# Optimization experiments

Hardware: AMD Instinct MI355X
Metric: run time of the kernel (lower is better)

The kernel has to match this reference:

```python
import jax, jax.numpy as jnp
import numpy as np

B, C_IN, C_OUT, T, R, CO = 8, 64, 64, 32, 32, 32


def setup_inputs() -> dict:
    key = jax.random.key(0)
    ks = jax.random.split(key, 8)
    scale = 1.0 / np.sqrt(C_IN)  # nn.Linear default uniform(-1/sqrt(in), 1/sqrt(in))
    w = lambda k: jax.random.uniform(k, (C_OUT, C_IN), jnp.float32, -scale, scale)
    return {
        "x": jax.random.normal(ks[0], (B, C_IN, T, R, CO), jnp.float32),
        "w_self": w(ks[1]),
        "w_tp": w(ks[2]),
        "w_tm": w(ks[3]),
        "w_rp": w(ks[4]),
        "w_rm": w(ks[5]),
        "w_cp": w(ks[6]),
        "w_cm": w(ks[7]),
    }


def _proj(v, w):
    # v: [B, t, r, c, C_in], w: [C_out, C_in] (nn.Linear layout)
    return jnp.einsum('btrci,oi->btrco', v, w)


def _shift_pad(a, axis, front):
    # pad 1 slice at front (True) or back (False) along `axis` of a 5-D tensor
    pads = [(0, 0)] * 5
    pads[axis] = (1, 0) if front else (0, 1)
    return jnp.pad(a, pads)


def reference(x, w_self, w_tp, w_tm, w_rp, w_rm, w_cp, w_cm):
    xp = jnp.transpose(x, (0, 2, 3, 4, 1))  # [B, T, R, Co, C_in]
    out = _proj(xp, w_self)
    if xp.shape[1] > 1:
        out = out + _shift_pad(_proj(xp[:, :-1], w_tp), 1, True)
        out = out + _shift_pad(_proj(xp[:, 1:], w_tm), 1, False)
    if xp.shape[2] > 1:
        out = out + _shift_pad(_proj(xp[:, :, :-1], w_rp), 2, True)
        out = out + _shift_pad(_proj(xp[:, :, 1:], w_rm), 2, False)
    if xp.shape[3] > 1:
        out = out + _shift_pad(_proj(xp[:, :, :, :-1], w_cp), 3, True)
        out = out + _shift_pad(_proj(xp[:, :, :, 1:], w_cm), 3, False)
    return jnp.transpose(out, (0, 4, 1, 2, 3))  # [B, C_out, T, R, Co]
```

## Files before the change

kernel.cpp:

```cpp
#include <hip/hip_runtime.h>


#define SB 32768
#define CIN 64
#define COUT 64
#define NB 8

typedef short s16x8 __attribute__((ext_vector_type(8)));
typedef __bf16 bf16x8 __attribute__((ext_vector_type(8)));
typedef float f32x4 __attribute__((ext_vector_type(4)));

__device__ __forceinline__ unsigned f2bf(float f) {
    unsigned u = __float_as_uint(f);
    u += 0x7FFFu + ((u >> 16) & 1u);
    return u >> 16;
}
__device__ __forceinline__ unsigned pk2(float lo, float hi) {
    return f2bf(lo) | (f2bf(hi) << 16);
}

__global__ __launch_bounds__(256) void wprep_kernel(const float* __restrict__ w0,
                            const float* __restrict__ w1, const float* __restrict__ w2,
                            const float* __restrict__ w3, const float* __restrict__ w4,
                            const float* __restrict__ w5, const float* __restrict__ w6,
                            unsigned short* __restrict__ ws) {
    int tap = blockIdx.x;
    int tid = threadIdx.x;
    const float* w = (tap == 0) ? w0 : (tap == 1) ? w1 : (tap == 2) ? w2
                   : (tap == 3) ? w3 : (tap == 4) ? w4 : (tap == 5) ? w5 : w6;
    unsigned p[8];
#pragma unroll
    for (int j = 0; j < 8; ++j)
        p[j] = pk2(w[tid * 16 + 2 * j], w[tid * 16 + 2 * j + 1]);
    uint4* dp = (uint4*)(ws + tap * 4096 + tid * 16);
    dp[0] = make_uint4(p[0], p[1], p[2], p[3]);
    dp[1] = make_uint4(p[4], p[5], p[6], p[7]);
}

__global__ __launch_bounds__(256) void conv_kernel(const float* __restrict__ x,
                                                   const unsigned short* __restrict__ wq,
                                                   float* __restrict__ out) {
    __shared__ uint4 alds[1536];
    int bid = blockIdx.x;
    int b = bid >> 8;
    int sblk = (bid & 255) << 7;
    int tid = threadIdx.x;
    const float* xb = x + (size_t)b * CIN * SB;

    {
        int row = tid & 127;
        int half = tid >> 7;
        int rl = 32 + row;
        const float* xp = xb + sblk + row + (size_t)(half * 32) * SB;
        unsigned pk[16];
#pragma unroll
        for (int u = 0; u < 16; ++u)
            pk[u] = pk2(xp[(size_t)(2 * u) * SB], xp[(size_t)(2 * u + 1) * SB]);
#pragma unroll
        for (int j = 0; j < 4; ++j)
            alds[rl * 8 + ((half * 4 + j) ^ (rl & 7))] =
                make_uint4(pk[4 * j], pk[4 * j + 1], pk[4 * j + 2], pk[4 * j + 3]);
    }
    {
        int hrow = tid & 63;
        int rl = (hrow < 32) ? hrow : hrow + 128;
        int s = sblk - 32 + rl;
        s = max(0, min(SB - 1, s));
        int ic = tid >> 6;
        const float* xp = xb + s + (size_t)(ic * 16) * SB;
        unsigned pk[8];
#pragma unroll
        for (int u = 0; u < 8; ++u)
            pk[u] = pk2(xp[(size_t)(2 * u) * SB], xp[(size_t)(2 * u + 1) * SB]);
        alds[rl * 8 + ((2 * ic) ^ (rl & 7))] = make_uint4(pk[0], pk[1], pk[2], pk[3]);
        alds[rl * 8 + ((2 * ic + 1) ^ (rl & 7))] = make_uint4(pk[4], pk[5], pk[6], pk[7]);
    }
    __syncthreads();

    int lane = tid & 63;
    int wv = tid >> 6;
    int lo = lane & 15;
    int quad = lane >> 4;
    int sbase = sblk + wv * 32;
    int t = sblk >> 10;

    f32x4 acc[2][4];
#pragma unroll
    for (int mt = 0; mt < 2; ++mt)
#pragma unroll
        for (int nt = 0; nt < 4; ++nt)
            acc[mt][nt] = (f32x4){0.f, 0.f, 0.f, 0.f};

    int r_m[2], c_m[2], rl[2];
#pragma unroll
    for (int mt = 0; mt < 2; ++mt) {
        int s = sbase + mt * 16 + lo;
        r_m[mt] = (s >> 5) & 31;
        c_m[mt] = s & 31;
        rl[mt] = s - sblk + 32;
    }

    auto load_b = [&](const unsigned short* wt, int ks, int nt) -> bf16x8 {
        const unsigned short* bp = wt + (nt * 16 + lo) * 64 + ks * 32 + quad * 8;
        return __builtin_bit_cast(bf16x8, *(const s16x8*)bp);
    };

    auto run_tap_lds = [&](int tap, int d, const bool ok[2]) {
        const unsigned short* wt = wq + tap * 4096;
#pragma unroll
        for (int ks = 0; ks < 2; ++ks) {
            bf16x8 bf[4];
#pragma unroll
            for (int nt = 0; nt < 4; ++nt) bf[nt] = load_b(wt, ks, nt);
            int j = ks * 4 + quad;
#pragma unroll
            for (int mt = 0; mt < 2; ++mt) {
                int row = rl[mt] + d;
                s16x8 raw = *((const s16x8*)alds + row * 8 + (j ^ (row & 7)));
                s16x8 zz = {0, 0, 0, 0, 0, 0, 0, 0};
                raw = ok[mt] ? raw : zz;
                bf16x8 af = __builtin_bit_cast(bf16x8, raw);
#pragma unroll
                for (int nt = 0; nt < 4; ++nt)
                    acc[mt][nt] = __builtin_amdgcn_mfma_f32_16x16x32_bf16(af, bf[nt], acc[mt][nt], 0, 0, 0);
            }
        }
    };

    auto run_tap_gather = [&](int tap, int d) {
        const unsigned short* wt = wq + tap * 4096;
#pragma unroll
        for (int ks = 0; ks < 2; ++ks) {
            bf16x8 bf[4];
#pragma unroll
            for (int nt = 0; nt < 4; ++nt) bf[nt] = load_b(wt, ks, nt);
            const float* gp = xb + (size_t)(ks * 32 + quad * 8) * SB + d;
#pragma unroll
            for (int mt = 0; mt < 2; ++mt) {
                const float* ap = gp + sbase + mt * 16 + lo;
                unsigned pk[4];
#pragma unroll
                for (int u = 0; u < 4; ++u)
                    pk[u] = pk2(ap[(size_t)(2 * u) * SB], ap[(size_t)(2 * u + 1) * SB]);
                uint4 v = make_uint4(pk[0], pk[1], pk[2], pk[3]);
                bf16x8 af = __builtin_bit_cast(bf16x8, v);
#pragma unroll
                for (int nt = 0; nt < 4; ++nt)
                    acc[mt][nt] = __builtin_amdgcn_mfma_f32_16x16x32_bf16(af, bf[nt], acc[mt][nt], 0, 0, 0);
            }
        }
    };

    {
        bool ok_all[2] = {true, true};
        run_tap_lds(0, 0, ok_all);
    }
    if (t > 0)  run_tap_gather(1, -1024);
    if (t < 31) run_tap_gather(2, 1024);
    {
        bool ok[2];
#pragma unroll
        for (int mt = 0; mt < 2; ++mt) ok[mt] = (r_m[mt] > 0);
        run_tap_lds(3, -32, ok);
#pragma unroll
        for (int mt = 0; mt < 2; ++mt) ok[mt] = (r_m[mt] < 31);
        run_tap_lds(4, 32, ok);
#pragma unroll
        for (int mt = 0; mt < 2; ++mt) ok[mt] = (c_m[mt] > 0);
        run_tap_lds(5, -1, ok);
#pragma unroll
        for (int mt = 0; mt < 2; ++mt) ok[mt] = (c_m[mt] < 31);
        run_tap_lds(6, 1, ok);
    }

#pragma unroll
    for (int mt = 0; mt < 2; ++mt) {
#pragma unroll
        for (int nt = 0; nt < 4; ++nt) {
            int o = nt * 16 + lo;
            size_t off = ((size_t)(b * COUT + o)) * SB + sbase + mt * 16 + quad * 4;
            *(f32x4*)(out + off) = acc[mt][nt];
        }
    }
}

__global__ void fallback_kernel(const float* __restrict__ x,
                                const float* __restrict__ w0, const float* __restrict__ w1,
                                const float* __restrict__ w2, const float* __restrict__ w3,
                                const float* __restrict__ w4, const float* __restrict__ w5,
                                const float* __restrict__ w6,
                                float* __restrict__ out) {
    int bid = blockIdx.x;
    int b = bid >> 11;
    int og = (bid >> 7) & 15;
    int sblk = (bid & 127) << 8;
    int tid = threadIdx.x;
    __shared__ float wl[7][4][64];
    const float* wp[7] = {w0, w1, w2, w3, w4, w5, w6};
    for (int k = tid; k < 7 * 4 * 64; k += 256) {
        int tap = k >> 8, oo = (k >> 6) & 3, i = k & 63;
        wl[tap][oo][i] = wp[tap][(og * 4 + oo) * 64 + i];
    }
    __syncthreads();
    int s = sblk + tid;
    int t = s >> 10, r = (s >> 5) & 31, c = s & 31;
    const float* xb = x + (size_t)b * CIN * SB + s;
    float a0 = 0, a1 = 0, a2 = 0, a3 = 0;
    for (int i = 0; i < 64; ++i) {
        const float* xi = xb + (size_t)i * SB;
        float vs = xi[0];
        float vtp = (t > 0) ? xi[-1024] : 0.f;
        float vtm = (t < 31) ? xi[1024] : 0.f;
        float vrp = (r > 0) ? xi[-32] : 0.f;
        float vrm = (r < 31) ? xi[32] : 0.f;
        float vcp = (c > 0) ? xi[-1] : 0.f;
        float vcm = (c < 31) ? xi[1] : 0.f;
        a0 += wl[0][0][i] * vs + wl[1][0][i] * vtp + wl[2][0][i] * vtm + wl[3][0][i] * vrp + wl[4][0][i] * vrm + wl[5][0][i] * vcp + wl[6][0][i] * vcm;
        a1 += wl[0][1][i] * vs + wl[1][1][i] * vtp + wl[2][1][i] * vtm + wl[3][1][i] * vrp + wl[4][1][i] * vrm + wl[5][1][i] * vcp + wl[6][1][i] * vcm;
        a2 += wl[0][2][i] * vs + wl[1][2][i] * vtp + wl[2][2][i] * vtm + wl[3][2][i] * vrp + wl[4][2][i] * vrm + wl[5][2][i] * vcp + wl[6][2][i] * vcm;
        a3 += wl[0][3][i] * vs + wl[1][3][i] * vtp + wl[2][3][i] * vtm + wl[3][3][i] * vrp + wl[4][3][i] * vrm + wl[5][3][i] * vcp + wl[6][3][i] * vcm;
    }
    size_t obase = ((size_t)b * COUT + og * 4) * SB + s;
    out[obase] = a0;
    out[obase + SB] = a1;
    out[obase + 2 * (size_t)SB] = a2;
    out[obase + 3 * (size_t)SB] = a3;
}

extern "C" void kernel_launch(void* const* d_in, const int* in_sizes, int n_in,
                              void* d_out, int out_size, void* d_ws, size_t ws_size,
                              hipStream_t stream) {
    const float* x = (const float*)d_in[0];
    const float* w0 = (const float*)d_in[1];
    const float* w1 = (const float*)d_in[2];
    const float* w2 = (const float*)d_in[3];
    const float* w3 = (const float*)d_in[4];
    const float* w4 = (const float*)d_in[5];
    const float* w5 = (const float*)d_in[6];
    const float* w6 = (const float*)d_in[7];
    float* out = (float*)d_out;

    size_t need = (size_t)7 * 4096 * 2;
    if (d_ws != nullptr && ws_size >= need) {
        unsigned short* wsp = (unsigned short*)d_ws;
        wprep_kernel<<<7, 256, 0, stream>>>(w0, w1, w2, w3, w4, w5, w6, wsp);
        conv_kernel<<<2048, 256, 0, stream>>>(x, wsp, out);
    } else {
        fallback_kernel<<<8 * 16 * 128, 256, 0, stream>>>(x, w0, w1, w2, w3, w4, w5, w6, out);
    }
}
```

Before: 182.0 us.

## Stage T-neighbor slabs in LDS and load x with float2 vector reads

```diff
diff --git a/kernel.cpp b/kernel.cpp
--- a/kernel.cpp
+++ b/kernel.cpp
@@ -40,40 +40,41 @@
 __global__ __launch_bounds__(256) void conv_kernel(const float* __restrict__ x,
                                                    const unsigned short* __restrict__ wq,
                                                    float* __restrict__ out) {
-    __shared__ uint4 alds[1536];
+    __shared__ uint4 alds[3584];
     int bid = blockIdx.x;
     int b = bid >> 8;
-    int sblk = (bid & 255) << 7;
+    int t = (bid >> 3) & 31;
+    int sbw = bid & 7;
+    int sblk = t * 1024 + sbw * 128;
     int tid = threadIdx.x;
     const float* xb = x + (size_t)b * CIN * SB;
 
     {
-        int row = tid & 127;
-        int half = tid >> 7;
-        int rl = 32 + row;
-        const float* xp = xb + sblk + row + (size_t)(half * 32) * SB;
-        unsigned pk[16];
-#pragma unroll
-        for (int u = 0; u < 16; ++u)
-            pk[u] = pk2(xp[(size_t)(2 * u) * SB], xp[(size_t)(2 * u + 1) * SB]);
-#pragma unroll
-        for (int j = 0; j < 4; ++j)
-            alds[rl * 8 + ((half * 4 + j) ^ (rl & 7))] =
-                make_uint4(pk[4 * j], pk[4 * j + 1], pk[4 * j + 2], pk[4 * j + 3]);
-    }
-    {
-        int hrow = tid & 63;
-        int rl = (hrow < 32) ? hrow : hrow + 128;
-        int s = sblk - 32 + rl;
-        s = max(0, min(SB - 1, s));
-        int ic = tid >> 6;
-        const float* xp = xb + s + (size_t)(ic * 16) * SB;
-        unsigned pk[8];
-#pragma unroll
-        for (int u = 0; u < 8; ++u)
-            pk[u] = pk2(xp[(size_t)(2 * u) * SB], xp[(size_t)(2 * u + 1) * SB]);
-        alds[rl * 8 + ((2 * ic) ^ (rl & 7))] = make_uint4(pk[0], pk[1], pk[2], pk[3]);
-        alds[rl * 8 + ((2 * ic + 1) ^ (rl & 7))] = make_uint4(pk[4], pk[5], pk[6], pk[7]);
+        int rl0 = 2 * tid;
+        if (rl0 < 448) {
+            int s0;
+            if (rl0 < 192)      s0 = sblk - 32 + rl0;
+            else if (rl0 < 320) s0 = sblk - 1024 + (rl0 - 192);
+            else                s0 = sblk + 1024 + (rl0 - 320);
+            s0 = max(0, min(SB - 2, s0));
+            const float* xp = xb + s0;
+            int sw = tid & 7;
+#pragma unroll
+            for (int j = 0; j < 8; ++j) {
+                float2 f[8];
+#pragma unroll
+                for (int c = 0; c < 8; ++c)
+                    f[c] = *(const float2*)(xp + (size_t)(j * 8 + c) * SB);
+                unsigned e0[4], e1[4];
+#pragma unroll
+                for (int p = 0; p < 4; ++p) {
+                    e0[p] = pk2(f[2 * p].x, f[2 * p + 1].x);
+                    e1[p] = pk2(f[2 * p].y, f[2 * p + 1].y);
+                }
+                alds[(size_t)rl0 * 8 + (j ^ sw)] = make_uint4(e0[0], e0[1], e0[2], e0[3]);
+                alds[(size_t)(rl0 + 1) * 8 + (j ^ sw)] = make_uint4(e1[0], e1[1], e1[2], e1[3]);
+            }
+        }
     }
     __syncthreads();
 
@@ -82,7 +83,6 @@
     int lo = lane & 15;
     int quad = lane >> 4;
     int sbase = sblk + wv * 32;
-    int t = sblk >> 10;
 
     f32x4 acc[2][4];
 #pragma unroll
@@ -91,13 +91,13 @@
         for (int nt = 0; nt < 4; ++nt)
             acc[mt][nt] = (f32x4){0.f, 0.f, 0.f, 0.f};
 
-    int r_m[2], c_m[2], rl[2];
+    int r_m[2], c_m[2], rlc[2];
 #pragma unroll
     for (int mt = 0; mt < 2; ++mt) {
         int s = sbase + mt * 16 + lo;
         r_m[mt] = (s >> 5) & 31;
         c_m[mt] = s & 31;
-        rl[mt] = s - sblk + 32;
+        rlc[mt] = (s - sblk) + 32;
     }
 
     auto load_b = [&](const unsigned short* wt, int ks, int nt) -> bf16x8 {
@@ -105,7 +105,7 @@
         return __builtin_bit_cast(bf16x8, *(const s16x8*)bp);
     };
 
-    auto run_tap_lds = [&](int tap, int d, const bool ok[2]) {
+    auto run_tap = [&](int tap, int d, const bool ok[2]) {
         const unsigned short* wt = wq + tap * 4096;
 #pragma unroll
         for (int ks = 0; ks < 2; ++ks) {
@@ -115,8 +115,8 @@
             int j = ks * 4 + quad;
 #pragma unroll
             for (int mt = 0; mt < 2; ++mt) {
-                int row = rl[mt] + d;
-                s16x8 raw = *((const s16x8*)alds + row * 8 + (j ^ (row & 7)));
+                int row = rlc[mt] + d;
+                s16x8 raw = *((const s16x8*)alds + (size_t)row * 8 + (j ^ ((row >> 1) & 7)));
                 s16x8 zz = {0, 0, 0, 0, 0, 0, 0, 0};
                 raw = ok[mt] ? raw : zz;
                 bf16x8 af = __builtin_bit_cast(bf16x8, raw);
@@ -127,50 +127,24 @@
         }
     };
 
-    auto run_tap_gather = [&](int tap, int d) {
-        const unsigned short* wt = wq + tap * 4096;
-#pragma unroll
-        for (int ks = 0; ks < 2; ++ks) {
-            bf16x8 bf[4];
-#pragma unroll
-            for (int nt = 0; nt < 4; ++nt) bf[nt] = load_b(wt, ks, nt);
-            const float* gp = xb + (size_t)(ks * 32 + quad * 8) * SB + d;
-#pragma unroll
-            for (int mt = 0; mt < 2; ++mt) {
-                const float* ap = gp + sbase + mt * 16 + lo;
-                unsigned pk[4];
-#pragma unroll
-                for (int u = 0; u < 4; ++u)
-                    pk[u] = pk2(ap[(size_t)(2 * u) * SB], ap[(size_t)(2 * u + 1) * SB]);
-                uint4 v = make_uint4(pk[0], pk[1], pk[2], pk[3]);
-                bf16x8 af = __builtin_bit_cast(bf16x8, v);
-#pragma unroll
-                for (int nt = 0; nt < 4; ++nt)
-                    acc[mt][nt] = __builtin_amdgcn_mfma_f32_16x16x32_bf16(af, bf[nt], acc[mt][nt], 0, 0, 0);
-            }
-        }
-    };
-
-    {
-        bool ok_all[2] = {true, true};
-        run_tap_lds(0, 0, ok_all);
-    }
-    if (t > 0)  run_tap_gather(1, -1024);
-    if (t < 31) run_tap_gather(2, 1024);
+    bool ok_all[2] = {true, true};
+    run_tap(0, 0, ok_all);
+    if (t > 0)  run_tap(1, 160, ok_all);
+    if (t < 31) run_tap(2, 288, ok_all);
     {
         bool ok[2];
 #pragma unroll
         for (int mt = 0; mt < 2; ++mt) ok[mt] = (r_m[mt] > 0);
-        run_tap_lds(3, -32, ok);
+        run_tap(3, -32, ok);
 #pragma unroll
         for (int mt = 0; mt < 2; ++mt) ok[mt] = (r_m[mt] < 31);
-        run_tap_lds(4, 32, ok);
+        run_tap(4, 32, ok);
 #pragma unroll
         for (int mt = 0; mt < 2; ++mt) ok[mt] = (c_m[mt] > 0);
-        run_tap_lds(5, -1, ok);
+        run_tap(5, -1, ok);
 #pragma unroll
         for (int mt = 0; mt < 2; ++mt) ok[mt] = (c_m[mt] < 31);
-        run_tap_lds(6, 1, ok);
+        run_tap(6, 1, ok);
     }
 
 #pragma unroll
```

Result: slower. 186.9 us (+2.7%).
